# Kernel optimization log

Hardware: AMD Instinct MI355X
Metric: run time of the kernel (lower is better)

Reference implementation:

```python
import jax, jax.numpy as jnp
import numpy as np

N_HEADS = 8
NEG_INF = -1e9


def setup_inputs() -> dict:
    key = jax.random.key(0)
    ks = jax.random.split(key, 9)
    B, S, D = 4, 2048, 512
    scale = 1.0 / np.sqrt(D)
    x = jax.random.normal(ks[0], (B, S, D), dtype=jnp.float32)
    mask = jnp.tril(jnp.ones((S, S), dtype=bool))[None, None, :, :]  # causal [1,1,S,S]
    W_Q_w = jax.random.normal(ks[1], (D, D), dtype=jnp.float32) * scale
    W_Q_b = jax.random.normal(ks[2], (D,), dtype=jnp.float32) * 0.02
    W_K_w = jax.random.normal(ks[3], (D, D), dtype=jnp.float32) * scale
    W_K_b = jax.random.normal(ks[4], (D,), dtype=jnp.float32) * 0.02
    W_V_w = jax.random.normal(ks[5], (D, D), dtype=jnp.float32) * scale
    W_V_b = jax.random.normal(ks[6], (D,), dtype=jnp.float32) * 0.02
    W_O_w = jax.random.normal(ks[7], (D, D), dtype=jnp.float32) * scale
    W_O_b = jax.random.normal(ks[8], (D,), dtype=jnp.float32) * 0.02
    return {"x": x, "mask": mask,
            "W_Q_w": W_Q_w, "W_Q_b": W_Q_b, "W_K_w": W_K_w, "W_K_b": W_K_b,
            "W_V_w": W_V_w, "W_V_b": W_V_b, "W_O_w": W_O_w, "W_O_b": W_O_b}


def reference(x, mask, W_Q_w, W_Q_b, W_K_w, W_K_b, W_V_w, W_V_b, W_O_w, W_O_b):
    B, S, D = x.shape
    H = N_HEADS
    Dh = D // H
    # projections (torch Linear: x @ W.T + b), split heads -> [B,H,S,Dh]
    def split_heads(t):
        return t.reshape(B, S, H, Dh).transpose(0, 2, 1, 3)
    Q = split_heads(x @ W_Q_w.T + W_Q_b)
    K = split_heads(x @ W_K_w.T + W_K_b)
    V = split_heads(x @ W_V_w.T + W_V_b)
    # scaled dot-product attention with explicit [B,H,S,S] scores
    scores = jnp.einsum("bhqd,bhkd->bhqk", Q, K) / jnp.sqrt(jnp.float32(Dh))
    scores = jnp.where(mask, scores, jnp.float32(NEG_INF))
    att = jax.nn.softmax(scores, axis=-1)
    out = jnp.einsum("bhqk,bhkd->bhqd", att, V)
    out = out.transpose(0, 2, 1, 3).reshape(B, S, D)
    return out @ W_O_w.T + W_O_b
```

## Files before the change

kernel.cpp:

```cpp
#include <hip/hip_runtime.h>
#include <hip/hip_bf16.h>

#define BATCH 4
#define SEQ   2048
#define DIM   512
#define NH    8
#define DH    64
#define NTOK  (BATCH*SEQ)

typedef __bf16 bf16x8 __attribute__((ext_vector_type(8)));
typedef float  f32x4  __attribute__((ext_vector_type(4)));

#define MFMA16(a,b,c) __builtin_amdgcn_mfma_f32_16x16x32_bf16((a),(b),(c),0,0,0)

#if __has_builtin(__builtin_amdgcn_exp2f)
#define EXP2F(x) __builtin_amdgcn_exp2f(x)
#else
#define EXP2F(x) exp2f(x)
#endif

#define QSCALE 0.18033688011112042f
#define SMAX 16.0f

typedef __attribute__((address_space(1))) void GAS;
typedef __attribute__((address_space(3))) void LAS;
__device__ __forceinline__ void gl_lds16(const void* g, void* l) {
  __builtin_amdgcn_global_load_lds((GAS*)g, (LAS*)l, 16, 0, 0);
}

__global__ __launch_bounds__(256) void cvt_all(
    const float* __restrict__ x,
    const float* __restrict__ s0, const float* __restrict__ s1,
    const float* __restrict__ s2, const float* __restrict__ s3,
    __bf16* __restrict__ xb,
    __bf16* __restrict__ o0, __bf16* __restrict__ o1,
    __bf16* __restrict__ o2, __bf16* __restrict__ o3) {
  const int i = blockIdx.x * 256 + threadIdx.x;
  const float* src;
  __bf16* dst;
  int off;
  if (i < 524288) {
    src = x; dst = xb; off = i;
  } else {
    const int j = i - 524288;
    const int which = j >> 15; off = j & 32767;
    src = (which == 0) ? s0 : (which == 1) ? s1 : (which == 2) ? s2 : s3;
    dst = (which == 0) ? o0 : (which == 1) ? o1 : (which == 2) ? o2 : o3;
  }
  const float4* s = (const float4*)src;
  float4 a = s[2*off], b = s[2*off+1];
  bf16x8 o;
  o[0] = (__bf16)a.x; o[1] = (__bf16)a.y; o[2] = (__bf16)a.z; o[3] = (__bf16)a.w;
  o[4] = (__bf16)b.x; o[5] = (__bf16)b.y; o[6] = (__bf16)b.z; o[7] = (__bf16)b.w;
  *(bf16x8*)&dst[8*off] = o;
}

__global__ __launch_bounds__(256) void gemm_qkv(
    const __bf16* __restrict__ xb,
    const __bf16* __restrict__ wq, const __bf16* __restrict__ wk,
    const __bf16* __restrict__ wv,
    const float* __restrict__ bq, const float* __restrict__ bk,
    const float* __restrict__ bv,
    __bf16* __restrict__ Qb, __bf16* __restrict__ Kb, __bf16* __restrict__ Vt)
{
  const int z = blockIdx.z;
  const __bf16* W    = (z == 0) ? wq : (z == 1) ? wk : wv;
  const float*  bias = (z == 0) ? bq : (z == 1) ? bk : bv;

  __shared__ __align__(16) __bf16 smem[128*152];
  __bf16* As = smem;
  __bf16* Bs = smem + 128*64;

  const int tid  = threadIdx.x;
  const int m0   = blockIdx.x * 128, n0 = blockIdx.y * 128;
  const int w    = tid >> 6, lane = tid & 63, quad = lane >> 4, l16 = lane & 15;
  const int wm   = (w >> 1) * 64, wn = (w & 1) * 64;
  const int srow = w*32 + (lane >> 3);
  const int scc  = (lane & 7) * 8;

  f32x4 acc[4][4] = {};

  for (int k0 = 0; k0 < DIM; k0 += 64) {
#pragma unroll
    for (int i = 0; i < 4; ++i) {
      const int row = srow + i*8;
      gl_lds16(&xb[(size_t)(m0+row)*DIM + k0 + scc], &As[(w*4+i)*512]);
      gl_lds16(&W [(size_t)(n0+row)*DIM + k0 + scc], &Bs[(w*4+i)*512]);
    }
    __syncthreads();
#pragma unroll
    for (int kk = 0; kk < 2; ++kk) {
      const int ko = kk*32 + quad*8;
      bf16x8 af[4], bfr[4];
#pragma unroll
      for (int f = 0; f < 4; ++f) {
        af[f]  = *(const bf16x8*)&As[(wm + f*16 + l16)*64 + ko];
        bfr[f] = *(const bf16x8*)&Bs[(wn + f*16 + l16)*64 + ko];
      }
#pragma unroll
      for (int fm = 0; fm < 4; ++fm)
#pragma unroll
        for (int fn = 0; fn < 4; ++fn)
          acc[fm][fn] = MFMA16(af[fm], bfr[fn], acc[fm][fn]);
    }
    __syncthreads();
  }

  __bf16* Cs = smem;
#pragma unroll
  for (int fm = 0; fm < 4; ++fm) {
#pragma unroll
    for (int fn = 0; fn < 4; ++fn) {
      const int cl  = wn + fn*16 + l16;
      const float bc = bias[n0 + cl];
#pragma unroll
      for (int r = 0; r < 4; ++r) {
        const int rl = wm + fm*16 + quad*4 + r;
        float v = acc[fm][fn][r] + bc;
        if (z == 0) v *= QSCALE;
        Cs[rl*152 + cl] = (__bf16)v;
      }
    }
  }
  __syncthreads();

  if (z < 2) {
    const int r  = tid >> 1, hh = tid & 1;
    const int grow = m0 + r, b = grow >> 11, s = grow & 2047;
    const int h  = (n0 >> 6) + hh;
    __bf16* O = (z == 0) ? Qb : Kb;
    __bf16* dst = O + ((size_t)(b*NH + h)*SEQ + s)*DH;
    const __bf16* srcr = &Cs[r*152 + hh*64];
#pragma unroll
    for (int j = 0; j < 8; ++j)
      *(bf16x8*)&dst[j*8] = *(const bf16x8*)&srcr[j*8];
  } else {
    const int c  = tid >> 1, hh = tid & 1;
    const int col = n0 + c, h = col >> 6, dh = col & 63;
    const int b  = m0 >> 11, sbase = (m0 & 2047) + hh*64;
    __bf16* dst = Vt + ((size_t)(b*NH + h)*DH + dh)*SEQ + sbase;
#pragma unroll
    for (int j8 = 0; j8 < 8; ++j8) {
      bf16x8 o;
#pragma unroll
      for (int e = 0; e < 8; ++e)
        o[e] = Cs[(hh*64 + j8*8 + e)*152 + c];
      *(bf16x8*)&dst[j8*8] = o;
    }
  }
}

__global__ __launch_bounds__(256) void gemm_out(
    const __bf16* __restrict__ attnb, const __bf16* __restrict__ wo,
    const float* __restrict__ bo, float* __restrict__ out)
{
  __shared__ __align__(16) __bf16 As[64*64];
  __shared__ __align__(16) __bf16 Bs[128*64];

  const int tid = threadIdx.x;
  const int m0  = blockIdx.x * 64, n0 = blockIdx.y * 128;
  const int w   = tid >> 6, lane = tid & 63, quad = lane >> 4, l16 = lane & 15;
  const int wm  = (w >> 1) * 32, wn = (w & 1) * 64;
  const int srow = w*8 + (lane >> 3);
  const int scc  = (lane & 7) * 8;

  f32x4 acc[2][4] = {};

  for (int k0 = 0; k0 < DIM; k0 += 64) {
#pragma unroll
    for (int i = 0; i < 2; ++i)
      gl_lds16(&attnb[(size_t)(m0 + srow + i*32)*DIM + k0 + scc],
               &As[(i*4 + w)*512]);
#pragma unroll
    for (int i = 0; i < 4; ++i)
      gl_lds16(&wo[(size_t)(n0 + srow + i*32)*DIM + k0 + scc],
               &Bs[(i*4 + w)*512]);
    __syncthreads();
#pragma unroll
    for (int kk = 0; kk < 2; ++kk) {
      const int ko = kk*32 + quad*8;
      bf16x8 af[2], bfr[4];
#pragma unroll
      for (int f = 0; f < 2; ++f)
        af[f]  = *(const bf16x8*)&As[(wm + f*16 + l16)*64 + ko];
#pragma unroll
      for (int f = 0; f < 4; ++f)
        bfr[f] = *(const bf16x8*)&Bs[(wn + f*16 + l16)*64 + ko];
#pragma unroll
      for (int fm = 0; fm < 2; ++fm)
#pragma unroll
        for (int fn = 0; fn < 4; ++fn)
          acc[fm][fn] = MFMA16(af[fm], bfr[fn], acc[fm][fn]);
    }
    __syncthreads();
  }

#pragma unroll
  for (int fm = 0; fm < 2; ++fm) {
#pragma unroll
    for (int fn = 0; fn < 4; ++fn) {
      const int col  = n0 + wn + fn*16 + l16;
      const float bc = bo[col];
#pragma unroll
      for (int r = 0; r < 4; ++r) {
        const int row = m0 + wm + fm*16 + quad*4 + r;
        out[(size_t)row*DIM + col] = acc[fm][fn][r] + bc;
      }
    }
  }
}

__global__ __launch_bounds__(64) void flash_attn(
    const __bf16* __restrict__ Qb, const __bf16* __restrict__ Kb,
    const __bf16* __restrict__ Vt, __bf16* __restrict__ attnb)
{
  const int idx = blockIdx.x;
  const int bh  = idx & 31;
  const int t   = 63 - (idx >> 5);
  const int b   = bh >> 3, h = bh & 7;
  const int lane = threadIdx.x & 63, quad = lane >> 4, l16 = lane & 15;
  const int q0  = t * 32;

  const __bf16* Qp = Qb + (size_t)bh * SEQ * DH;
  const __bf16* Kp = Kb + (size_t)bh * SEQ * DH;
  const __bf16* Vp = Vt + (size_t)bh * DH * SEQ;

  __shared__ __align__(16) __bf16 Pw[32*136];

  bf16x8 qf[2][2];
#pragma unroll
  for (int mf = 0; mf < 2; ++mf)
#pragma unroll
    for (int kk = 0; kk < 2; ++kk)
      qf[mf][kk] = *(const bf16x8*)&Qp[(size_t)(q0 + mf*16 + l16)*DH + kk*32 + quad*8];

  f32x4 of[2][4] = {};
  float l_[2][4];
#pragma unroll
  for (int mf = 0; mf < 2; ++mf)
#pragma unroll
    for (int r = 0; r < 4; ++r) l_[mf][r] = 0.f;

  const int nsteps = (q0 + 32 + 127) >> 7;

  bf16x8 kf[8][2];
#pragma unroll
  for (int fn = 0; fn < 8; ++fn)
#pragma unroll
    for (int kk = 0; kk < 2; ++kk)
      kf[fn][kk] = *(const bf16x8*)&Kp[(size_t)(fn*16 + l16)*DH + kk*32 + quad*8];

  for (int kt = 0; kt < nsteps; ++kt) {
    const int k0 = kt * 128;

    bf16x8 vf[4][4];
#pragma unroll
    for (int nd = 0; nd < 4; ++nd)
#pragma unroll
      for (int kq = 0; kq < 2; ++kq)
        vf[nd][kq] = *(const bf16x8*)&Vp[(size_t)(nd*16 + l16)*SEQ + k0 +
                                         kq*32 + quad*8];

    f32x4 sf[2][8] = {};
    __builtin_amdgcn_s_setprio(1);
#pragma unroll
    for (int mf = 0; mf < 2; ++mf)
#pragma unroll
      for (int fn = 0; fn < 8; ++fn) {
        sf[mf][fn] = MFMA16(qf[mf][0], kf[fn][0], sf[mf][fn]);
        sf[mf][fn] = MFMA16(qf[mf][1], kf[fn][1], sf[mf][fn]);
      }
    __builtin_amdgcn_s_setprio(0);

    {
      const int kn0 = (kt + 1 < nsteps) ? k0 + 128 : 0;
#pragma unroll
      for (int fn = 0; fn < 8; ++fn)
#pragma unroll
        for (int kk = 0; kk < 2; ++kk)
          kf[fn][kk] = *(const bf16x8*)&Kp[(size_t)(kn0 + fn*16 + l16)*DH +
                                           kk*32 + quad*8];
    }

    if (k0 + 127 > q0) {
#pragma unroll
      for (int mf = 0; mf < 2; ++mf)
#pragma unroll
        for (int fn = 0; fn < 8; ++fn) {
          const int col = k0 + fn*16 + l16;
#pragma unroll
          for (int r = 0; r < 4; ++r) {
            const int row = q0 + mf*16 + quad*4 + r;
            if (col > row) sf[mf][fn][r] = -1e30f;
          }
        }
    }

#pragma unroll
    for (int fn = 0; fn < 8; ++fn)
#pragma unroll
      for (int r = 0; r < 4; ++r) {
        const float p = EXP2F(sf[0][fn][r] - SMAX);
        l_[0][r] += p;
        Pw[(quad*4 + r)*136 + fn*16 + l16] = (__bf16)p;
      }

#pragma unroll
    for (int nd = 0; nd < 4; ++nd)
#pragma unroll
      for (int kq = 2; kq < 4; ++kq)
        vf[nd][kq] = *(const bf16x8*)&Vp[(size_t)(nd*16 + l16)*SEQ + k0 +
                                         kq*32 + quad*8];

#pragma unroll
    for (int fn = 0; fn < 8; ++fn)
#pragma unroll
      for (int r = 0; r < 4; ++r) {
        const float p = EXP2F(sf[1][fn][r] - SMAX);
        l_[1][r] += p;
        Pw[(16 + quad*4 + r)*136 + fn*16 + l16] = (__bf16)p;
      }

    __builtin_amdgcn_s_setprio(1);
#pragma unroll
    for (int kq = 0; kq < 4; ++kq) {
      const bf16x8 pa0 = *(const bf16x8*)&Pw[(l16)*136 + kq*32 + quad*8];
      const bf16x8 pa1 = *(const bf16x8*)&Pw[(16 + l16)*136 + kq*32 + quad*8];
#pragma unroll
      for (int nd = 0; nd < 4; ++nd) {
        of[0][nd] = MFMA16(pa0, vf[nd][kq], of[0][nd]);
        of[1][nd] = MFMA16(pa1, vf[nd][kq], of[1][nd]);
      }
    }
    __builtin_amdgcn_s_setprio(0);
  }

#pragma unroll
  for (int d = 1; d < 16; d <<= 1)
#pragma unroll
    for (int mf = 0; mf < 2; ++mf)
#pragma unroll
      for (int r = 0; r < 4; ++r)
        l_[mf][r] += __shfl_xor(l_[mf][r], d);
#pragma unroll
  for (int mf = 0; mf < 2; ++mf)
#pragma unroll
    for (int r = 0; r < 4; ++r)
      l_[mf][r] = 1.0f / l_[mf][r];
#pragma unroll
  for (int mf = 0; mf < 2; ++mf)
#pragma unroll
    for (int nd = 0; nd < 4; ++nd) {
      const int dh = nd*16 + l16;
#pragma unroll
      for (int r = 0; r < 4; ++r) {
        const int q = q0 + mf*16 + quad*4 + r;
        attnb[((size_t)b*SEQ + q)*DIM + h*DH + dh] = (__bf16)(of[mf][nd][r] * l_[mf][r]);
      }
    }
}

extern "C" void kernel_launch(void* const* d_in, const int* in_sizes, int n_in,
                              void* d_out, int out_size, void* d_ws, size_t ws_size,
                              hipStream_t stream) {
  const float* x  = (const float*)d_in[0];
  const float* Wq = (const float*)d_in[2];
  const float* bq = (const float*)d_in[3];
  const float* Wk = (const float*)d_in[4];
  const float* bk = (const float*)d_in[5];
  const float* Wv = (const float*)d_in[6];
  const float* bv = (const float*)d_in[7];
  const float* Wo = (const float*)d_in[8];
  const float* bo = (const float*)d_in[9];
  float* out = (float*)d_out;

  __bf16* xb    = (__bf16*)d_ws;
  __bf16* wq    = xb + (size_t)NTOK*DIM;
  __bf16* wk    = wq + DIM*DIM;
  __bf16* wv    = wk + DIM*DIM;
  __bf16* wo    = wv + DIM*DIM;
  __bf16* Qb    = wo + DIM*DIM;
  __bf16* Kb    = Qb + (size_t)NTOK*DIM;
  __bf16* Vt    = Kb + (size_t)NTOK*DIM;
  __bf16* attnb = Vt + (size_t)NTOK*DIM;

  cvt_all<<<2560, 256, 0, stream>>>(x, Wq, Wk, Wv, Wo, xb, wq, wk, wv, wo);

  gemm_qkv<<<dim3(NTOK/128, DIM/128, 3), 256, 0, stream>>>(
      xb, wq, wk, wv, bq, bk, bv, Qb, Kb, Vt);

  flash_attn<<<2048, 64, 0, stream>>>(Qb, Kb, Vt, attnb);

  gemm_out<<<dim3(NTOK/64, DIM/128), 256, 0, stream>>>(attnb, wo, bo, out);
}
```

Measured before the change: 204.6 us.

## Share K/V tiles in LDS across eight query-tile waves per block

The attention kernel moves from 2048 single-wave blocks to 256 blocks of 8 waves. Each block's waves handle strided query tiles of one (batch, head) and share 64-key K/V tiles staged cooperatively in LDS, with a register prefetch of the next tile. This cuts redundant global K/V loads. In exchange it adds two block barriers per key tile, and waves that have finished their causal range sit idle until the block's longest tile is done. It also uses fewer blocks, which may hurt occupancy and load balance across CUs.

After: 183.3 us. 1.12x faster.

```diff
diff --git a/kernel.cpp b/kernel.cpp
--- a/kernel.cpp
+++ b/kernel.cpp
@@ -210,22 +210,32 @@
   }
 }
 
-__global__ __launch_bounds__(64) void flash_attn(
+__global__ __launch_bounds__(512) void flash_attn(
     const __bf16* __restrict__ Qb, const __bf16* __restrict__ Kb,
     const __bf16* __restrict__ Vt, __bf16* __restrict__ attnb)
 {
   const int idx = blockIdx.x;
   const int bh  = idx & 31;
-  const int t   = 63 - (idx >> 5);
+  const int j   = idx >> 5;
   const int b   = bh >> 3, h = bh & 7;
-  const int lane = threadIdx.x & 63, quad = lane >> 4, l16 = lane & 15;
+  const int tid = threadIdx.x;
+  const int w   = tid >> 6, lane = tid & 63, quad = lane >> 4, l16 = lane & 15;
+  const int t   = 8*w + j;
   const int q0  = t * 32;
+  const int myk = (q0 >> 6) + 1;
+  const int maxkt = ((56 + j) >> 1) + 1;
 
   const __bf16* Qp = Qb + (size_t)bh * SEQ * DH;
   const __bf16* Kp = Kb + (size_t)bh * SEQ * DH;
   const __bf16* Vp = Vt + (size_t)bh * DH * SEQ;
 
-  __shared__ __align__(16) __bf16 Pw[32*136];
+  __shared__ __align__(16) __bf16 Ks[64*72];
+  __shared__ __align__(16) __bf16 Vs[64*72];
+  __shared__ __align__(16) __bf16 Pall[8*32*72];
+  __bf16* Pw = Pall + w*(32*72);
+
+  const int srow = tid >> 3;
+  const int scol = (tid & 7) * 8;
 
   bf16x8 qf[2][2];
 #pragma unroll
@@ -241,98 +251,90 @@
 #pragma unroll
     for (int r = 0; r < 4; ++r) l_[mf][r] = 0.f;
 
-  const int nsteps = (q0 + 32 + 127) >> 7;
-
-  bf16x8 kf[8][2];
-#pragma unroll
-  for (int fn = 0; fn < 8; ++fn)
-#pragma unroll
-    for (int kk = 0; kk < 2; ++kk)
-      kf[fn][kk] = *(const bf16x8*)&Kp[(size_t)(fn*16 + l16)*DH + kk*32 + quad*8];
-
-  for (int kt = 0; kt < nsteps; ++kt) {
-    const int k0 = kt * 128;
-
-    bf16x8 vf[4][4];
-#pragma unroll
-    for (int nd = 0; nd < 4; ++nd)
-#pragma unroll
-      for (int kq = 0; kq < 2; ++kq)
-        vf[nd][kq] = *(const bf16x8*)&Vp[(size_t)(nd*16 + l16)*SEQ + k0 +
-                                         kq*32 + quad*8];
-
-    f32x4 sf[2][8] = {};
-    __builtin_amdgcn_s_setprio(1);
-#pragma unroll
-    for (int mf = 0; mf < 2; ++mf)
-#pragma unroll
-      for (int fn = 0; fn < 8; ++fn) {
-        sf[mf][fn] = MFMA16(qf[mf][0], kf[fn][0], sf[mf][fn]);
-        sf[mf][fn] = MFMA16(qf[mf][1], kf[fn][1], sf[mf][fn]);
-      }
-    __builtin_amdgcn_s_setprio(0);
-
-    {
-      const int kn0 = (kt + 1 < nsteps) ? k0 + 128 : 0;
-#pragma unroll
-      for (int fn = 0; fn < 8; ++fn)
+  {
+    bf16x8 kr = *(const bf16x8*)&Kp[(size_t)srow*DH + scol];
+    bf16x8 vr = *(const bf16x8*)&Vp[(size_t)srow*SEQ + scol];
+    *(bf16x8*)&Ks[srow*72 + scol] = kr;
+    *(bf16x8*)&Vs[srow*72 + scol] = vr;
+  }
+  __syncthreads();
+
+  for (int kt = 0; kt < maxkt; ++kt) {
+    const int k0 = kt * 64;
+    const int kn0 = (kt + 1 < maxkt) ? k0 + 64 : 0;
+    bf16x8 kr = *(const bf16x8*)&Kp[(size_t)(kn0 + srow)*DH + scol];
+    bf16x8 vr = *(const bf16x8*)&Vp[(size_t)srow*SEQ + kn0 + scol];
+
+    if (kt < myk) {
+      bf16x8 kf[4][2], vf[4][2];
+#pragma unroll
+      for (int fn = 0; fn < 4; ++fn)
 #pragma unroll
         for (int kk = 0; kk < 2; ++kk)
-          kf[fn][kk] = *(const bf16x8*)&Kp[(size_t)(kn0 + fn*16 + l16)*DH +
-                                           kk*32 + quad*8];
-    }
-
-    if (k0 + 127 > q0) {
+          kf[fn][kk] = *(const bf16x8*)&Ks[(fn*16 + l16)*72 + kk*32 + quad*8];
+#pragma unroll
+      for (int nd = 0; nd < 4; ++nd)
+#pragma unroll
+        for (int kq = 0; kq < 2; ++kq)
+          vf[nd][kq] = *(const bf16x8*)&Vs[(nd*16 + l16)*72 + kq*32 + quad*8];
+
+      f32x4 sf[2][4] = {};
+      __builtin_amdgcn_s_setprio(1);
 #pragma unroll
       for (int mf = 0; mf < 2; ++mf)
 #pragma unroll
-        for (int fn = 0; fn < 8; ++fn) {
-          const int col = k0 + fn*16 + l16;
+        for (int fn = 0; fn < 4; ++fn) {
+          sf[mf][fn] = MFMA16(qf[mf][0], kf[fn][0], sf[mf][fn]);
+          sf[mf][fn] = MFMA16(qf[mf][1], kf[fn][1], sf[mf][fn]);
+        }
+      __builtin_amdgcn_s_setprio(0);
+
+      if (k0 + 63 > q0) {
+#pragma unroll
+        for (int mf = 0; mf < 2; ++mf)
+#pragma unroll
+          for (int fn = 0; fn < 4; ++fn) {
+            const int col = k0 + fn*16 + l16;
+#pragma unroll
+            for (int r = 0; r < 4; ++r) {
+              const int row = q0 + mf*16 + quad*4 + r;
+              if (col > row) sf[mf][fn][r] = -1e30f;
+            }
+          }
+      }
+
+#pragma unroll
+      for (int mf = 0; mf < 2; ++mf)
+#pragma unroll
+        for (int fn = 0; fn < 4; ++fn)
 #pragma unroll
           for (int r = 0; r < 4; ++r) {
-            const int row = q0 + mf*16 + quad*4 + r;
-            if (col > row) sf[mf][fn][r] = -1e30f;
+            const float p = EXP2F(sf[mf][fn][r] - SMAX);
+            l_[mf][r] += p;
+            Pw[(mf*16 + quad*4 + r)*72 + fn*16 + l16] = (__bf16)p;
           }
+
+      bf16x8 pa[2][2];
+#pragma unroll
+      for (int mf = 0; mf < 2; ++mf)
+#pragma unroll
+        for (int kq = 0; kq < 2; ++kq)
+          pa[mf][kq] = *(const bf16x8*)&Pw[(mf*16 + l16)*72 + kq*32 + quad*8];
+      __builtin_amdgcn_s_setprio(1);
+#pragma unroll
+      for (int mf = 0; mf < 2; ++mf)
+#pragma unroll
+        for (int nd = 0; nd < 4; ++nd) {
+          of[mf][nd] = MFMA16(pa[mf][0], vf[nd][0], of[mf][nd]);
+          of[mf][nd] = MFMA16(pa[mf][1], vf[nd][1], of[mf][nd]);
         }
-    }
-
-#pragma unroll
-    for (int fn = 0; fn < 8; ++fn)
-#pragma unroll
-      for (int r = 0; r < 4; ++r) {
-        const float p = EXP2F(sf[0][fn][r] - SMAX);
-        l_[0][r] += p;
-        Pw[(quad*4 + r)*136 + fn*16 + l16] = (__bf16)p;
-      }
-
-#pragma unroll
-    for (int nd = 0; nd < 4; ++nd)
-#pragma unroll
-      for (int kq = 2; kq < 4; ++kq)
-        vf[nd][kq] = *(const bf16x8*)&Vp[(size_t)(nd*16 + l16)*SEQ + k0 +
-                                         kq*32 + quad*8];
-
-#pragma unroll
-    for (int fn = 0; fn < 8; ++fn)
-#pragma unroll
-      for (int r = 0; r < 4; ++r) {
-        const float p = EXP2F(sf[1][fn][r] - SMAX);
-        l_[1][r] += p;
-        Pw[(16 + quad*4 + r)*136 + fn*16 + l16] = (__bf16)p;
-      }
-
-    __builtin_amdgcn_s_setprio(1);
-#pragma unroll
-    for (int kq = 0; kq < 4; ++kq) {
-      const bf16x8 pa0 = *(const bf16x8*)&Pw[(l16)*136 + kq*32 + quad*8];
-      const bf16x8 pa1 = *(const bf16x8*)&Pw[(16 + l16)*136 + kq*32 + quad*8];
-#pragma unroll
-      for (int nd = 0; nd < 4; ++nd) {
-        of[0][nd] = MFMA16(pa0, vf[nd][kq], of[0][nd]);
-        of[1][nd] = MFMA16(pa1, vf[nd][kq], of[1][nd]);
-      }
-    }
-    __builtin_amdgcn_s_setprio(0);
+      __builtin_amdgcn_s_setprio(0);
+    }
+
+    __syncthreads();
+    *(bf16x8*)&Ks[srow*72 + scol] = kr;
+    *(bf16x8*)&Vs[srow*72 + scol] = vr;
+    __syncthreads();
   }
 
 #pragma unroll
@@ -389,7 +391,7 @@
   gemm_qkv<<<dim3(NTOK/128, DIM/128, 3), 256, 0, stream>>>(
       xb, wq, wk, wv, bq, bk, bv, Qb, Kb, Vt);
 
-  flash_attn<<<2048, 64, 0, stream>>>(Qb, Kb, Vt, attnb);
+  flash_attn<<<256, 512, 0, stream>>>(Qb, Kb, Vt, attnb);
 
   gemm_out<<<dim3(NTOK/64, DIM/128), 256, 0, stream>>>(attnb, wo, bo, out);
 }
```
